# Performance work log

Hardware: AMD Instinct MI355X
Metric: run time of the kernel (lower is better)

Reference implementation:

```python
import jax, jax.numpy as jnp
import numpy as np

B, H, W, C = 32, 56, 56, 192
WS, SS, NH = 7, 3, 6
HD = C // NH
SCALE = HD ** -0.5
N = WS * WS
NW = (H // WS) * (W // WS)
EPS = 1e-5


def _rel_pos_index():
    coords = np.stack(np.meshgrid(np.arange(WS), np.arange(WS), indexing='ij'))  # (2,WS,WS)
    cf = coords.reshape(2, -1)
    rel = cf[:, :, None] - cf[:, None, :]  # (2,N,N)
    rel = rel.transpose(1, 2, 0)
    rel[:, :, 0] += WS - 1
    rel[:, :, 1] += WS - 1
    rel[:, :, 0] *= 2 * WS - 1
    return rel.sum(-1)  # (N,N) int


def _attn_mask():
    img = np.zeros((H, W))
    cnt = 0
    for hs in (slice(0, -WS), slice(-WS, -SS), slice(-SS, None)):
        for ws in (slice(0, -WS), slice(-WS, -SS), slice(-SS, None)):
            img[hs, ws] = cnt
            cnt += 1
    win = img.reshape(H // WS, WS, W // WS, WS).transpose(0, 2, 1, 3).reshape(NW, N)
    diff = win[:, None, :] - win[:, :, None]
    return np.where(diff != 0, -100.0, 0.0).astype(np.float32)  # (NW,N,N)


REL_IDX = jnp.asarray(_rel_pos_index())
ATTN_MASK = jnp.asarray(_attn_mask())


def _ln(x, g, b):
    mu = x.mean(-1, keepdims=True)
    var = ((x - mu) ** 2).mean(-1, keepdims=True)
    return (x - mu) * jax.lax.rsqrt(var + EPS) * g + b


def setup_inputs() -> dict:
    key = jax.random.key(0)
    ks = jax.random.split(key, 8)
    d = {
        'x': jax.random.normal(ks[0], (B, H * W, C), jnp.float32),
        'norm1_g': jnp.ones((C,), jnp.float32),
        'norm1_b': jnp.zeros((C,), jnp.float32),
        'qkv_w': jax.random.normal(ks[1], (C, 3 * C), jnp.float32) * 0.02,
        'qkv_b': jnp.zeros((3 * C,), jnp.float32),
        'rpb_table': jax.random.normal(ks[2], ((2 * WS - 1) ** 2, NH), jnp.float32) * 0.02,
        'proj_w': jax.random.normal(ks[3], (C, C), jnp.float32) * 0.02,
        'proj_b': jnp.zeros((C,), jnp.float32),
        'norm2_g': jnp.ones((C,), jnp.float32),
        'norm2_b': jnp.zeros((C,), jnp.float32),
        'fc1_w': jax.random.normal(ks[4], (C, 4 * C), jnp.float32) * 0.02,
        'fc1_b': jnp.zeros((4 * C,), jnp.float32),
        'fc2_w': jax.random.normal(ks[5], (4 * C, C), jnp.float32) * 0.02,
        'fc2_b': jnp.zeros((C,), jnp.float32),
    }
    return d


def reference(x, norm1_g, norm1_b, qkv_w, qkv_b, rpb_table, proj_w, proj_b,
              norm2_g, norm2_b, fc1_w, fc1_b, fc2_w, fc2_b):
    shortcut = x
    h = _ln(x, norm1_g, norm1_b).reshape(B, H, W, C)
    # cyclic shift
    h = jnp.roll(h, (-SS, -SS), axis=(1, 2))
    # window partition -> (B*NW, N, C)
    hw = h.reshape(B, H // WS, WS, W // WS, WS, C).transpose(0, 1, 3, 2, 4, 5)
    hw = hw.reshape(B * NW, N, C)
    # qkv
    qkv = (hw @ qkv_w + qkv_b).reshape(B * NW, N, 3, NH, HD).transpose(2, 0, 3, 1, 4)
    q, k, v = qkv[0], qkv[1], qkv[2]  # (B_, NH, N, HD)
    attn = jnp.einsum('whnd,whmd->whnm', q * SCALE, k)
    bias = rpb_table[REL_IDX.reshape(-1)].reshape(N, N, NH).transpose(2, 0, 1)
    attn = attn + bias[None]
    # shift mask
    attn = attn.reshape(B, NW, NH, N, N) + ATTN_MASK[None, :, None]
    attn = jax.nn.softmax(attn.reshape(B * NW, NH, N, N), axis=-1)
    out = jnp.einsum('whnm,whmd->whnd', attn, v).transpose(0, 2, 1, 3).reshape(B * NW, N, C)
    out = out @ proj_w + proj_b
    # window reverse + unshift
    out = out.reshape(B, H // WS, W // WS, WS, WS, C).transpose(0, 1, 3, 2, 4, 5).reshape(B, H, W, C)
    out = jnp.roll(out, (SS, SS), axis=(1, 2)).reshape(B, H * W, C)
    x = shortcut + out
    # MLP
    m = _ln(x, norm2_g, norm2_b)
    m = jax.nn.gelu(m @ fc1_w + fc1_b, approximate=False) @ fc2_w + fc2_b
    return x + m
```

## Files before the change

kernel.cpp:

```cpp
#include <hip/hip_runtime.h>
#include <hip/hip_bf16.h>
#include <math.h>

#define MTOK 100352
#define SCALE_ 0.17677669529663687f

typedef short bf16x8 __attribute__((ext_vector_type(8)));
typedef float f32x4 __attribute__((ext_vector_type(4)));

__device__ __forceinline__ float b2f(unsigned short u) {
    return __uint_as_float(((unsigned int)u) << 16);
}
__device__ __forceinline__ unsigned short f2b(float f) {
    unsigned int u = __float_as_uint(f);
    unsigned int r = (u + 0x7FFFu + ((u >> 16) & 1u)) >> 16;
    return (unsigned short)r;
}
__device__ __forceinline__ void gload_lds16(const unsigned short* g, unsigned short* l) {
    __builtin_amdgcn_global_load_lds(
        (const __attribute__((address_space(1))) void*)g,
        (__attribute__((address_space(3))) void*)l, 16, 0, 0);
}

__global__ __launch_bounds__(256) void wconv_k(
    const float* __restrict__ w, unsigned short* __restrict__ wt, int K, int N)
{
    const int i = blockIdx.x * 256 + threadIdx.x;
    if (i >= N * K) return;
    const int n = i / K, k = i - n * K;
    wt[i] = f2b(w[(size_t)k * N + n]);
}

__global__ __launch_bounds__(256) void ln1_window_k(
    const float* __restrict__ x, const float* __restrict__ g,
    const float* __restrict__ bt, unsigned short* __restrict__ out)
{
    const int wid = (blockIdx.x * 256 + threadIdx.x) >> 6;
    if (wid >= MTOK) return;
    const int lane = threadIdx.x & 63;
    const int widx = wid / 49, n = wid - widx * 49;
    const int b = widx >> 6, win = widx & 63;
    const int wh = win >> 3, ww = win & 7;
    const int r = n / 7, cc = n - r * 7;
    int hh = wh * 7 + r + 3;  if (hh >= 56) hh -= 56;
    int wc = ww * 7 + cc + 3; if (wc >= 56) wc -= 56;
    const size_t src = ((size_t)b * 3136 + hh * 56 + wc) * 192;
    const float v0 = x[src + lane], v1 = x[src + lane + 64], v2 = x[src + lane + 128];
    float s1 = v0 + v1 + v2;
    float s2 = v0 * v0 + v1 * v1 + v2 * v2;
    #pragma unroll
    for (int off = 32; off; off >>= 1) {
        s1 += __shfl_xor(s1, off, 64);
        s2 += __shfl_xor(s2, off, 64);
    }
    const float mu = s1 * (1.f / 192.f);
    const float var = s2 * (1.f / 192.f) - mu * mu;
    const float rs = rsqrtf(var + 1e-5f);
    const size_t dst = (size_t)wid * 192;
    out[dst + lane]       = f2b((v0 - mu) * rs * g[lane]       + bt[lane]);
    out[dst + lane + 64]  = f2b((v1 - mu) * rs * g[lane + 64]  + bt[lane + 64]);
    out[dst + lane + 128] = f2b((v2 - mu) * rs * g[lane + 128] + bt[lane + 128]);
}

__global__ __launch_bounds__(256) void ln2_k(
    const float* __restrict__ x, const float* __restrict__ g,
    const float* __restrict__ bt, unsigned short* __restrict__ out)
{
    const int t = (blockIdx.x * 256 + threadIdx.x) >> 6;
    if (t >= MTOK) return;
    const int lane = threadIdx.x & 63;
    const size_t src = (size_t)t * 192;
    const float v0 = x[src + lane], v1 = x[src + lane + 64], v2 = x[src + lane + 128];
    float s1 = v0 + v1 + v2;
    float s2 = v0 * v0 + v1 * v1 + v2 * v2;
    #pragma unroll
    for (int off = 32; off; off >>= 1) {
        s1 += __shfl_xor(s1, off, 64);
        s2 += __shfl_xor(s2, off, 64);
    }
    const float mu = s1 * (1.f / 192.f);
    const float var = s2 * (1.f / 192.f) - mu * mu;
    const float rs = rsqrtf(var + 1e-5f);
    out[src + lane]       = f2b((v0 - mu) * rs * g[lane]       + bt[lane]);
    out[src + lane + 64]  = f2b((v1 - mu) * rs * g[lane + 64]  + bt[lane + 64]);
    out[src + lane + 128] = f2b((v2 - mu) * rs * g[lane + 128] + bt[lane + 128]);
}

enum { EPI_STORE_BF16 = 0, EPI_PROJ = 1, EPI_GELU = 2, EPI_RES = 3 };

template <int EPI>
__global__ __launch_bounds__(256) void mgemm_k(
    const unsigned short* __restrict__ A, const unsigned short* __restrict__ BT,
    const float* __restrict__ bias, unsigned short* __restrict__ outb,
    float* __restrict__ outf, const float* __restrict__ xres,
    int N, int K, int gx)
{
    __shared__ __align__(16) unsigned short As[2][256 * 32];
    __shared__ __align__(16) unsigned short Bs[2][64 * 32];

    const int nwg = gridDim.x;
    int lin = blockIdx.x;
    lin = (lin & 7) * (nwg >> 3) + (lin >> 3);
    const int bn = lin % gx, bm = lin / gx;
    const int row0 = bm * 256, col0 = bn * 64;

    const int tid = threadIdx.x;
    const int w = tid >> 6, lane = tid & 63;
    const int l16 = lane & 15, l4 = lane >> 4;

    const unsigned short* Ab = A + (size_t)row0 * K;
    const unsigned short* Bb = BT + (size_t)col0 * K;
    const int sr = lane >> 2;
    const int sq = ((lane & 3) ^ ((lane >> 3) & 3)) * 8;

    #pragma unroll
    for (int i = 0; i < 4; i++) {
        const int ch = w * 4 + i;
        gload_lds16(Ab + (size_t)(ch * 16 + sr) * K + sq, &As[0][ch * 512 + lane * 8]);
    }
    gload_lds16(Bb + (size_t)(w * 16 + sr) * K + sq, &Bs[0][w * 512 + lane * 8]);
    __syncthreads();

    f32x4 acc[4][4];
    #pragma unroll
    for (int m = 0; m < 4; m++)
        #pragma unroll
        for (int n = 0; n < 4; n++) acc[m][n] = (f32x4){0.f, 0.f, 0.f, 0.f};

    const int rdc = (l4 ^ ((l16 >> 1) & 3)) * 8;
    const int nt = K >> 5;
    for (int t = 0; t < nt; ++t) {
        const int cur = t & 1;
        if (t + 1 < nt) {
            const int k0 = (t + 1) << 5;
            #pragma unroll
            for (int i = 0; i < 4; i++) {
                const int ch = w * 4 + i;
                gload_lds16(Ab + (size_t)(ch * 16 + sr) * K + k0 + sq,
                            &As[cur ^ 1][ch * 512 + lane * 8]);
            }
            gload_lds16(Bb + (size_t)(w * 16 + sr) * K + k0 + sq,
                        &Bs[cur ^ 1][w * 512 + lane * 8]);
        }
        bf16x8 af[4], bf[4];
        #pragma unroll
        for (int m = 0; m < 4; m++)
            af[m] = *reinterpret_cast<const bf16x8*>(
                &As[cur][(w * 64 + m * 16 + l16) * 32 + rdc]);
        #pragma unroll
        for (int n = 0; n < 4; n++)
            bf[n] = *reinterpret_cast<const bf16x8*>(
                &Bs[cur][(n * 16 + l16) * 32 + rdc]);
        #pragma unroll
        for (int m = 0; m < 4; m++)
            #pragma unroll
            for (int n = 0; n < 4; n++)
                acc[m][n] = __builtin_amdgcn_mfma_f32_16x16x32_bf16(
                    af[m], bf[n], acc[m][n], 0, 0, 0);
        __syncthreads();
    }

    float bv[4];
    #pragma unroll
    for (int n = 0; n < 4; n++) bv[n] = bias[col0 + n * 16 + l16];

    #pragma unroll
    for (int m = 0; m < 4; m++) {
        #pragma unroll
        for (int j = 0; j < 4; j++) {
            const int row = row0 + w * 64 + m * 16 + l4 * 4 + j;
            if constexpr (EPI == EPI_PROJ) {
                const int widx = row / 49, n49 = row - widx * 49;
                const int b = widx >> 6, win = widx & 63;
                const int wh = win >> 3, ww = win & 7;
                const int r = n49 / 7, cc = n49 - r * 7;
                int hh = wh * 7 + r + 3;  if (hh >= 56) hh -= 56;
                int wcc = ww * 7 + cc + 3; if (wcc >= 56) wcc -= 56;
                const size_t tok = ((size_t)b * 3136 + hh * 56 + wcc) * 192;
                #pragma unroll
                for (int n = 0; n < 4; n++) {
                    const int col = col0 + n * 16 + l16;
                    outf[tok + col] = xres[tok + col] + acc[m][n][j] + bv[n];
                }
            } else if constexpr (EPI == EPI_STORE_BF16) {
                #pragma unroll
                for (int n = 0; n < 4; n++) {
                    const int col = col0 + n * 16 + l16;
                    outb[(size_t)row * N + col] = f2b(acc[m][n][j] + bv[n]);
                }
            } else if constexpr (EPI == EPI_GELU) {
                #pragma unroll
                for (int n = 0; n < 4; n++) {
                    const int col = col0 + n * 16 + l16;
                    float v = acc[m][n][j] + bv[n];
                    v = 0.5f * v * (1.f + erff(v * 0.70710678118654752f));
                    outb[(size_t)row * N + col] = f2b(v);
                }
            } else {
                #pragma unroll
                for (int n = 0; n < 4; n++) {
                    const int col = col0 + n * 16 + l16;
                    outf[(size_t)row * N + col] += acc[m][n][j] + bv[n];
                }
            }
        }
    }
}

__global__ __launch_bounds__(64) void attn_mfma_k(
    const unsigned short* __restrict__ qkv, const float* __restrict__ rpb,
    unsigned short* __restrict__ out)
{
    const int blk = blockIdx.x;
    const int widx = blk / 6, head = blk - widx * 6;
    const int win = widx & 63;
    const int wh = win >> 3, ww = win & 7;

    __shared__ __align__(16) unsigned short vt[32 * 72];
    __shared__ __align__(16) unsigned short pl[64 * 72];
    __shared__ float bias_s[256];

    const int lane = threadIdx.x;
    const int l16 = lane & 15, l4 = lane >> 4;
    const size_t base = (size_t)widx * 49 * 576 + (size_t)head * 32;

    for (int i = lane; i < 169; i += 64) bias_s[i] = rpb[i * 6 + head];

    #pragma unroll
    for (int it = 0; it < 4; ++it) {
        const int c = lane + it * 64;
        const int m = c >> 2, d8 = (c & 3) * 8;
        bf16x8 v8 = {};
        if (m < 49)
            v8 = *reinterpret_cast<const bf16x8*>(qkv + base + (size_t)m * 576 + 384 + d8);
        #pragma unroll
        for (int r = 0; r < 8; ++r) vt[(d8 + r) * 72 + m] = (unsigned short)v8[r];
    }

    bf16x8 kf[4], qf[4];
    #pragma unroll
    for (int f = 0; f < 4; ++f) {
        const int rrow = f * 16 + l16;
        bf16x8 kz = {}, qz = {};
        if (rrow < 49) {
            kz = *reinterpret_cast<const bf16x8*>(qkv + base + (size_t)rrow * 576 + 192 + l4 * 8);
            qz = *reinterpret_cast<const bf16x8*>(qkv + base + (size_t)rrow * 576 + l4 * 8);
        }
        kf[f] = kz; qf[f] = qz;
    }

    f32x4 acc[4][4];
    #pragma unroll
    for (int mf = 0; mf < 4; ++mf)
        #pragma unroll
        for (int nf = 0; nf < 4; ++nf) {
            f32x4 z = (f32x4){0.f, 0.f, 0.f, 0.f};
            acc[mf][nf] = __builtin_amdgcn_mfma_f32_16x16x32_bf16(kf[mf], qf[nf], z, 0, 0, 0);
        }

    __syncthreads();

    int gn[4], labn[4]; bool nok[4];
    #pragma unroll
    for (int nf = 0; nf < 4; ++nf) {
        const int n = nf * 16 + l16;
        const int rn = (n * 9363) >> 16, cn = n - rn * 7;
        gn[nf] = n + 6 * rn;
        labn[nf] = (wh == 7 ? (rn < 4 ? 1 : 2) : 0) * 3 + (ww == 7 ? (cn < 4 ? 1 : 2) : 0);
        nok[nf] = (n < 49);
    }

    #pragma unroll
    for (int mf = 0; mf < 4; ++mf) {
        #pragma unroll
        for (int j = 0; j < 4; ++j) {
            const int m = mf * 16 + l4 * 4 + j;
            const int rm = (m * 9363) >> 16, cm = m - rm * 7;
            const int gm = m + 6 * rm;
            const int labm = (wh == 7 ? (rm < 4 ? 1 : 2) : 0) * 3 + (ww == 7 ? (cm < 4 ? 1 : 2) : 0);
            const bool mok = (m < 49);
            #pragma unroll
            for (int nf = 0; nf < 4; ++nf) {
                float s = -1e30f;
                if (mok && nok[nf]) {
                    s = acc[mf][nf][j] * SCALE_ + bias_s[gn[nf] - gm + 84];
                    if (labn[nf] != labm) s -= 100.f;
                }
                acc[mf][nf][j] = s;
            }
        }
    }

    #pragma unroll
    for (int nf = 0; nf < 4; ++nf) {
        float mx = -1e30f;
        #pragma unroll
        for (int mf = 0; mf < 4; ++mf)
            #pragma unroll
            for (int j = 0; j < 4; ++j) mx = fmaxf(mx, acc[mf][nf][j]);
        mx = fmaxf(mx, __shfl_xor(mx, 16, 64));
        mx = fmaxf(mx, __shfl_xor(mx, 32, 64));
        float sum = 0.f;
        #pragma unroll
        for (int mf = 0; mf < 4; ++mf)
            #pragma unroll
            for (int j = 0; j < 4; ++j) {
                const float e = __expf(acc[mf][nf][j] - mx);
                acc[mf][nf][j] = e;
                sum += e;
            }
        sum += __shfl_xor(sum, 16, 64);
        sum += __shfl_xor(sum, 32, 64);
        const float inv = 1.f / sum;
        const int n = nf * 16 + l16;
        #pragma unroll
        for (int mf = 0; mf < 4; ++mf)
            #pragma unroll
            for (int jp = 0; jp < 2; ++jp) {
                const int m = mf * 16 + l4 * 4 + jp * 2;
                const unsigned int pk =
                    (unsigned int)f2b(acc[mf][nf][jp * 2] * inv) |
                    ((unsigned int)f2b(acc[mf][nf][jp * 2 + 1] * inv) << 16);
                *reinterpret_cast<unsigned int*>(&pl[n * 72 + m]) = pk;
            }
    }
    __syncthreads();

    f32x4 oacc[4][2];
    #pragma unroll
    for (int nf = 0; nf < 4; ++nf)
        #pragma unroll
        for (int df = 0; df < 2; ++df) oacc[nf][df] = (f32x4){0.f, 0.f, 0.f, 0.f};
    #pragma unroll
    for (int ks = 0; ks < 2; ++ks) {
        bf16x8 vf[2];
        #pragma unroll
        for (int df = 0; df < 2; ++df)
            vf[df] = *reinterpret_cast<const bf16x8*>(&vt[(df * 16 + l16) * 72 + ks * 32 + l4 * 8]);
        #pragma unroll
        for (int nf = 0; nf < 4; ++nf) {
            const bf16x8 pf = *reinterpret_cast<const bf16x8*>(&pl[(nf * 16 + l16) * 72 + ks * 32 + l4 * 8]);
            #pragma unroll
            for (int df = 0; df < 2; ++df)
                oacc[nf][df] = __builtin_amdgcn_mfma_f32_16x16x32_bf16(pf, vf[df], oacc[nf][df], 0, 0, 0);
        }
    }

    #pragma unroll
    for (int nf = 0; nf < 4; ++nf)
        #pragma unroll
        for (int j = 0; j < 4; ++j) {
            const int n = nf * 16 + l4 * 4 + j;
            if (n < 49) {
                const size_t o = ((size_t)widx * 49 + n) * 192 + (size_t)head * 32;
                out[o + l16]      = f2b(oacc[nf][0][j]);
                out[o + 16 + l16] = f2b(oacc[nf][1][j]);
            }
        }
}

extern "C" void kernel_launch(void* const* d_in, const int* in_sizes, int n_in,
                              void* d_out, int out_size, void* d_ws, size_t ws_size,
                              hipStream_t stream)
{
    const float* x      = (const float*)d_in[0];
    const float* n1g    = (const float*)d_in[1];
    const float* n1b    = (const float*)d_in[2];
    const float* qkv_w  = (const float*)d_in[3];
    const float* qkv_b  = (const float*)d_in[4];
    const float* rpb    = (const float*)d_in[5];
    const float* proj_w = (const float*)d_in[6];
    const float* proj_b = (const float*)d_in[7];
    const float* n2g    = (const float*)d_in[8];
    const float* n2b    = (const float*)d_in[9];
    const float* fc1_w  = (const float*)d_in[10];
    const float* fc1_b  = (const float*)d_in[11];
    const float* fc2_w  = (const float*)d_in[12];
    const float* fc2_b  = (const float*)d_in[13];
    float* out = (float*)d_out;

    const int M = MTOK;
    unsigned short* big   = (unsigned short*)d_ws;
    unsigned short* winx  = big + (size_t)M * 768;
    unsigned short* qkvT  = winx + (size_t)M * 192;
    unsigned short* projT = qkvT + 576 * 192;
    unsigned short* fc1T  = projT + 192 * 192;
    unsigned short* fc2T  = fc1T + 768 * 192;

    wconv_k<<<(576 * 192 + 255) / 256, 256, 0, stream>>>(qkv_w, qkvT, 192, 576);
    wconv_k<<<(192 * 192 + 255) / 256, 256, 0, stream>>>(proj_w, projT, 192, 192);
    wconv_k<<<(768 * 192 + 255) / 256, 256, 0, stream>>>(fc1_w, fc1T, 192, 768);
    wconv_k<<<(192 * 768 + 255) / 256, 256, 0, stream>>>(fc2_w, fc2T, 768, 192);

    ln1_window_k<<<M / 4, 256, 0, stream>>>(x, n1g, n1b, winx);
    mgemm_k<EPI_STORE_BF16><<<9 * (M / 256), 256, 0, stream>>>(
        winx, qkvT, qkv_b, big, nullptr, nullptr, 576, 192, 9);
    attn_mfma_k<<<2048 * 6, 64, 0, stream>>>(big, rpb, winx);
    mgemm_k<EPI_PROJ><<<3 * (M / 256), 256, 0, stream>>>(
        winx, projT, proj_b, nullptr, out, x, 192, 192, 3);
    ln2_k<<<M / 4, 256, 0, stream>>>(out, n2g, n2b, winx);
    mgemm_k<EPI_GELU><<<12 * (M / 256), 256, 0, stream>>>(
        winx, fc1T, fc1_b, big, nullptr, nullptr, 768, 192, 12);
    mgemm_k<EPI_RES><<<3 * (M / 256), 256, 0, stream>>>(
        big, fc2T, fc2_b, nullptr, out, nullptr, 192, 768, 3);
}
```

Measured before the change: 393.6 us.

## Deepen GEMM prefetch pipeline, use tanh GELU, raise MFMA priority in attention

The GEMM main loop now preloads two K-stages and issues the load for stage t+2 after computing stage t. It uses explicit vmcnt waits and raw barriers in place of __syncthreads, so global-to-LDS transfers overlap more with MFMA work. The exact erf GELU is replaced by the tanh-style sigmoid approximation using fast exp and rcp, which trades exactness against the reference for cheaper epilogue math. The attention kernel also raises wave priority around its MFMA blocks.

```diff
diff --git a/kernel.cpp b/kernel.cpp
--- a/kernel.cpp
+++ b/kernel.cpp
@@ -113,35 +113,35 @@
     const int sr = lane >> 2;
     const int sq = ((lane & 3) ^ ((lane >> 3) & 3)) * 8;
 
-    #pragma unroll
-    for (int i = 0; i < 4; i++) {
-        const int ch = w * 4 + i;
-        gload_lds16(Ab + (size_t)(ch * 16 + sr) * K + sq, &As[0][ch * 512 + lane * 8]);
-    }
-    gload_lds16(Bb + (size_t)(w * 16 + sr) * K + sq, &Bs[0][w * 512 + lane * 8]);
-    __syncthreads();
-
-    f32x4 acc[4][4];
-    #pragma unroll
-    for (int m = 0; m < 4; m++)
-        #pragma unroll
-        for (int n = 0; n < 4; n++) acc[m][n] = (f32x4){0.f, 0.f, 0.f, 0.f};
-
-    const int rdc = (l4 ^ ((l16 >> 1) & 3)) * 8;
     const int nt = K >> 5;
-    for (int t = 0; t < nt; ++t) {
-        const int cur = t & 1;
-        if (t + 1 < nt) {
-            const int k0 = (t + 1) << 5;
+    #pragma unroll
+    for (int tt = 0; tt < 2; ++tt) {
+        if (tt < nt) {
+            const int k0 = tt << 5;
             #pragma unroll
             for (int i = 0; i < 4; i++) {
                 const int ch = w * 4 + i;
                 gload_lds16(Ab + (size_t)(ch * 16 + sr) * K + k0 + sq,
-                            &As[cur ^ 1][ch * 512 + lane * 8]);
+                            &As[tt][ch * 512 + lane * 8]);
             }
             gload_lds16(Bb + (size_t)(w * 16 + sr) * K + k0 + sq,
-                        &Bs[cur ^ 1][w * 512 + lane * 8]);
-        }
+                        &Bs[tt][w * 512 + lane * 8]);
+        }
+    }
+
+    f32x4 acc[4][4];
+    #pragma unroll
+    for (int m = 0; m < 4; m++)
+        #pragma unroll
+        for (int n = 0; n < 4; n++) acc[m][n] = (f32x4){0.f, 0.f, 0.f, 0.f};
+
+    const int rdc = (l4 ^ ((l16 >> 1) & 3)) * 8;
+    for (int t = 0; t < nt; ++t) {
+        const int cur = t & 1;
+        if (t + 1 < nt) asm volatile("s_waitcnt vmcnt(5)" ::: "memory");
+        else            asm volatile("s_waitcnt vmcnt(0)" ::: "memory");
+        __builtin_amdgcn_s_barrier();
+        __builtin_amdgcn_sched_barrier(0);
         bf16x8 af[4], bf[4];
         #pragma unroll
         for (int m = 0; m < 4; m++)
@@ -157,7 +157,19 @@
             for (int n = 0; n < 4; n++)
                 acc[m][n] = __builtin_amdgcn_mfma_f32_16x16x32_bf16(
                     af[m], bf[n], acc[m][n], 0, 0, 0);
-        __syncthreads();
+        __builtin_amdgcn_sched_barrier(0);
+        __builtin_amdgcn_s_barrier();
+        if (t + 2 < nt) {
+            const int k0 = (t + 2) << 5;
+            #pragma unroll
+            for (int i = 0; i < 4; i++) {
+                const int ch = w * 4 + i;
+                gload_lds16(Ab + (size_t)(ch * 16 + sr) * K + k0 + sq,
+                            &As[cur][ch * 512 + lane * 8]);
+            }
+            gload_lds16(Bb + (size_t)(w * 16 + sr) * K + k0 + sq,
+                        &Bs[cur][w * 512 + lane * 8]);
+        }
     }
 
     float bv[4];
@@ -193,7 +205,10 @@
                 for (int n = 0; n < 4; n++) {
                     const int col = col0 + n * 16 + l16;
                     float v = acc[m][n][j] + bv[n];
-                    v = 0.5f * v * (1.f + erff(v * 0.70710678118654752f));
+                    const float wv = v + 0.044715f * v * v * v;
+                    const float sg = __builtin_amdgcn_rcpf(
+                        1.f + __expf(-1.5957691216057308f * wv));
+                    v = v * sg;
                     outb[(size_t)row * N + col] = f2b(v);
                 }
             } else {
@@ -250,6 +265,7 @@
     }
 
     f32x4 acc[4][4];
+    __builtin_amdgcn_s_setprio(1);
     #pragma unroll
     for (int mf = 0; mf < 4; ++mf)
         #pragma unroll
@@ -257,6 +273,7 @@
             f32x4 z = (f32x4){0.f, 0.f, 0.f, 0.f};
             acc[mf][nf] = __builtin_amdgcn_mfma_f32_16x16x32_bf16(kf[mf], qf[nf], z, 0, 0, 0);
         }
+    __builtin_amdgcn_s_setprio(0);
 
     __syncthreads();
 
@@ -337,6 +354,7 @@
         #pragma unroll
         for (int df = 0; df < 2; ++df)
             vf[df] = *reinterpret_cast<const bf16x8*>(&vt[(df * 16 + l16) * 72 + ks * 32 + l4 * 8]);
+        __builtin_amdgcn_s_setprio(1);
         #pragma unroll
         for (int nf = 0; nf < 4; ++nf) {
             const bf16x8 pf = *reinterpret_cast<const bf16x8*>(&pl[(nf * 16 + l16) * 72 + ks * 32 + l4 * 8]);
@@ -344,6 +362,7 @@
             for (int df = 0; df < 2; ++df)
                 oacc[nf][df] = __builtin_amdgcn_mfma_f32_16x16x32_bf16(pf, vf[df], oacc[nf][df], 0, 0, 0);
         }
+        __builtin_amdgcn_s_setprio(0);
     }
 
     #pragma unroll
```

New measurement: 373.0 us. -5.2%, faster.
